# Optimization experiments

Hardware: AMD Instinct MI355X
Metric: run time of the kernel (lower is better)

## Reference

```python
import jax, jax.numpy as jnp
import numpy as np

NUM_HEADS = 16
DIM = 1280
HEAD_DIM = DIM // NUM_HEADS  # 80
N_TOKENS = 4096


def _rotate_half(x):
    x1, x2 = jnp.split(x, 2, axis=-1)
    return jnp.concatenate([-x2, x1], axis=-1)


def _apply_rotary_vision(t, freqs):
    # t: (N, H, D), freqs: (N, D//2)
    cos = jnp.tile(jnp.cos(freqs), (1, 2))[:, None, :]  # (N, 1, D)
    sin = jnp.tile(jnp.sin(freqs), (1, 2))[:, None, :]
    return t * cos + _rotate_half(t) * sin


def setup_inputs() -> dict:
    key = jax.random.key(0)
    ks = jax.random.split(key, 6)
    hidden_states = jax.random.normal(ks[0], (N_TOKENS, DIM), dtype=jnp.float32)
    # 4 packed variable-length image sequences
    cu_seqlens = jnp.array([0, 600, 1600, 2800, N_TOKENS], dtype=jnp.int32)
    rotary_pos_emb = jax.random.normal(ks[1], (N_TOKENS, HEAD_DIM // 2), dtype=jnp.float32)
    w_qkv = jax.random.normal(ks[2], (DIM, 3 * DIM), dtype=jnp.float32) * 0.02
    b_qkv = jax.random.normal(ks[3], (3 * DIM,), dtype=jnp.float32) * 0.02
    w_proj = jax.random.normal(ks[4], (DIM, DIM), dtype=jnp.float32) * 0.02
    b_proj = jax.random.normal(ks[5], (DIM,), dtype=jnp.float32) * 0.02
    return {"hidden_states": hidden_states, "cu_seqlens": cu_seqlens,
            "rotary_pos_emb": rotary_pos_emb, "w_qkv": w_qkv, "b_qkv": b_qkv,
            "w_proj": w_proj, "b_proj": b_proj}


def reference(hidden_states, cu_seqlens, rotary_pos_emb, w_qkv, b_qkv, w_proj, b_proj):
    N = hidden_states.shape[0]
    H, D = NUM_HEADS, HEAD_DIM
    qkv = hidden_states @ w_qkv + b_qkv                  # (N, 3*dim)
    qkv = qkv.reshape(N, 3, H, D)
    q, k, v = qkv[:, 0], qkv[:, 1], qkv[:, 2]            # (N, H, D)
    q = _apply_rotary_vision(q, rotary_pos_emb)
    k = _apply_rotary_vision(k, rotary_pos_emb)
    # segment id per token from cu_seqlens boundaries
    pos = jnp.arange(N, dtype=jnp.int32)
    seg = jnp.searchsorted(cu_seqlens, pos, side='right') - 1  # (N,)
    same_seg = seg[:, None] == seg[None, :]              # (N, N) bool
    scale = 1.0 / jnp.sqrt(jnp.asarray(D, dtype=q.dtype))
    scores = jnp.einsum('nhd,mhd->hnm', q, k) * scale    # (H, N, N)
    scores = jnp.where(same_seg[None, :, :], scores, jnp.finfo(scores.dtype).min)
    probs = jax.nn.softmax(scores, axis=-1)
    out = jnp.einsum('hnm,mhd->nhd', probs, v)           # (N, H, D)
    out = out.reshape(N, H * D)
    return out @ w_proj + b_proj
```

## Files before the change

### kernel.cpp

```cpp
#include <hip/hip_runtime.h>
#include <math.h>


#define N_TOK 4096
#define DIMM  1280
#define NHEAD 16
#define HD    80
#define QKVN  3840
#define KP    3840

typedef short bf16x8 __attribute__((ext_vector_type(8)));
typedef float f32x4  __attribute__((ext_vector_type(4)));

__device__ __forceinline__ unsigned short f2bf(float x) {
    unsigned int u = __float_as_uint(x);
    u += 0x7fff + ((u >> 16) & 1);
    return (unsigned short)(u >> 16);
}
__device__ __forceinline__ float bf2f(unsigned short h) {
    return __uint_as_float(((unsigned int)h) << 16);
}
__device__ __forceinline__ void gload_lds16(const void* g, void* l) {
    __builtin_amdgcn_global_load_lds(
        (const __attribute__((address_space(1))) unsigned int*)g,
        (__attribute__((address_space(3))) unsigned int*)l, 16, 0, 0);
}

#define MFMA16(a, b, c) __builtin_amdgcn_mfma_f32_16x16x32_bf16((a), (b), (c), 0, 0, 0)

__global__ void pack_A_kernel(const float* __restrict__ X, unsigned short* __restrict__ Ap)
{
    const int idx = blockIdx.x * blockDim.x + threadIdx.x;
    if (idx >= N_TOK * DIMM / 4) return;
    const int e = idx * 4;
    const int m = e / DIMM, k = e - (e / DIMM) * DIMM;
    const float4 v = *reinterpret_cast<const float4*>(&X[(size_t)m * DIMM + k]);
    ushort4 hi, lo;
    hi.x = f2bf(v.x); lo.x = f2bf(v.x - bf2f(hi.x));
    hi.y = f2bf(v.y); lo.y = f2bf(v.y - bf2f(hi.y));
    hi.z = f2bf(v.z); lo.z = f2bf(v.z - bf2f(hi.z));
    hi.w = f2bf(v.w); lo.w = f2bf(v.w - bf2f(hi.w));
    const size_t base = (size_t)m * KP + k;
    *reinterpret_cast<ushort4*>(&Ap[base])            = hi;
    *reinterpret_cast<ushort4*>(&Ap[base + DIMM])     = lo;
    *reinterpret_cast<ushort4*>(&Ap[base + 2 * DIMM]) = hi;
}

__global__ __launch_bounds__(256)
void pack_Bt_kernel(const float* __restrict__ W, unsigned short* __restrict__ Bt, int Ncols)
{
    __shared__ float Ts[32][33];
    const int k0 = blockIdx.x * 32, n0 = blockIdx.y * 32;
    const int t = threadIdx.x;
    const int r = t >> 3, c4 = (t & 7) * 4;
    const float4 v = *reinterpret_cast<const float4*>(&W[(size_t)(k0 + r) * Ncols + n0 + c4]);
    Ts[r][c4] = v.x; Ts[r][c4 + 1] = v.y; Ts[r][c4 + 2] = v.z; Ts[r][c4 + 3] = v.w;
    __syncthreads();
    float w0 = Ts[c4][r], w1 = Ts[c4 + 1][r], w2 = Ts[c4 + 2][r], w3 = Ts[c4 + 3][r];
    ushort4 hi, lo;
    hi.x = f2bf(w0); lo.x = f2bf(w0 - bf2f(hi.x));
    hi.y = f2bf(w1); lo.y = f2bf(w1 - bf2f(hi.y));
    hi.z = f2bf(w2); lo.z = f2bf(w2 - bf2f(hi.z));
    hi.w = f2bf(w3); lo.w = f2bf(w3 - bf2f(hi.w));
    const size_t base = (size_t)(n0 + r) * KP + k0 + c4;
    *reinterpret_cast<ushort4*>(&Bt[base])            = hi;
    *reinterpret_cast<ushort4*>(&Bt[base + DIMM])     = hi;
    *reinterpret_cast<ushort4*>(&Bt[base + 2 * DIMM]) = lo;
}

template<int EPI>
__global__ __launch_bounds__(256)
void gemm_mfma(const unsigned short* __restrict__ A, const unsigned short* __restrict__ Bt,
               const float* __restrict__ bias, float* __restrict__ out, int Ncols)
{
    __shared__ unsigned short As[128 * 32];
    __shared__ unsigned short Bs[128 * 32];

    const int tid  = threadIdx.x;
    const int w    = tid >> 6, lane = tid & 63;
    const int m0   = blockIdx.x * 128, n0 = blockIdx.y * 128;
    const int wm   = w >> 1, wn = w & 1;
    const int lm   = lane & 15, kb = lane >> 4;

    const char* Ag = (const char*)(A  + (size_t)(m0 + w * 32 + (lane >> 2)) * KP) + (lane & 3) * 16;
    const char* Bg = (const char*)(Bt + (size_t)(n0 + w * 32 + (lane >> 2)) * KP) + (lane & 3) * 16;
    char* AsB = (char*)As + w * 2048;
    char* BsB = (char*)Bs + w * 2048;
    const size_t rowskip = (size_t)16 * KP * 2;

    f32x4 acc[4][4] = {};

    for (int k0 = 0; k0 < KP; k0 += 32) {
        const size_t kb2 = (size_t)k0 * 2;
        gload_lds16(Ag + kb2,           AsB);
        gload_lds16(Ag + kb2 + rowskip, AsB + 1024);
        gload_lds16(Bg + kb2,           BsB);
        gload_lds16(Bg + kb2 + rowskip, BsB + 1024);
        __syncthreads();

        bf16x8 a[4], b[4];
        #pragma unroll
        for (int mf = 0; mf < 4; ++mf)
            a[mf] = *reinterpret_cast<const bf16x8*>(&As[(wm * 64 + mf * 16 + lm) * 32 + kb * 8]);
        #pragma unroll
        for (int nf = 0; nf < 4; ++nf)
            b[nf] = *reinterpret_cast<const bf16x8*>(&Bs[(wn * 64 + nf * 16 + lm) * 32 + kb * 8]);
        #pragma unroll
        for (int mf = 0; mf < 4; ++mf)
            #pragma unroll
            for (int nf = 0; nf < 4; ++nf)
                acc[mf][nf] = MFMA16(a[mf], b[nf], acc[mf][nf]);
        __syncthreads();
    }

    #pragma unroll
    for (int nf = 0; nf < 4; ++nf) {
        const int col = n0 + wn * 64 + nf * 16 + lm;
        const float bb = bias[col];
        #pragma unroll
        for (int mf = 0; mf < 4; ++mf) {
            #pragma unroll
            for (int r = 0; r < 4; ++r) {
                const int row = m0 + wm * 64 + mf * 16 + kb * 4 + r;
                const float c = acc[mf][nf][r] + bb;
                if (EPI == 0) {
                    out[(size_t)row * Ncols + col] = c;
                } else {
                    const int part = col / DIMM;
                    const int rem  = col - part * DIMM;
                    const int hh   = rem / HD;
                    const int d    = rem - hh * HD;
                    out[(((size_t)(part * NHEAD + hh)) * N_TOK + row) * HD + d] = c;
                }
            }
        }
    }
}

__global__ void rope_kernel(const float* __restrict__ freqs, float* __restrict__ q,
                            const float* __restrict__ k, unsigned short* __restrict__ Kp)
{
    const int idx = blockIdx.x * blockDim.x + threadIdx.x;
    if (idx >= N_TOK * NHEAD * 40) return;
    const int dp = idx % 40;
    const int t  = idx / 40;
    const int h  = t & 15;
    const int n  = t >> 4;

    const float f = freqs[n * 40 + dp];
    const float c = cosf(f);
    const float s = sinf(f);

    const size_t base = ((size_t)h * N_TOK + n) * HD;
    const float q1 = q[base + dp], q2 = q[base + dp + 40];
    q[base + dp]      = q1 * c - q2 * s;
    q[base + dp + 40] = q2 * c + q1 * s;

    const float scale = 0.11180339887498949f;
    const float k1 = k[base + dp], k2 = k[base + dp + 40];
    const float kr1 = (k1 * c - k2 * s) * scale;
    const float kr2 = (k2 * c + k1 * s) * scale;

    const size_t hi = ((size_t)(h * 2) * N_TOK + n) * 104;
    const size_t lo = ((size_t)(h * 2 + 1) * N_TOK + n) * 104;
    const unsigned short h1 = f2bf(kr1);
    Kp[hi + dp]      = h1;
    Kp[lo + dp]      = f2bf(kr1 - bf2f(h1));
    const unsigned short h2 = f2bf(kr2);
    Kp[hi + dp + 40] = h2;
    Kp[lo + dp + 40] = f2bf(kr2 - bf2f(h2));
    if (dp < 12) {
        Kp[hi + 80 + dp] = 0; Kp[hi + 92 + dp] = 0;
        Kp[lo + 80 + dp] = 0; Kp[lo + 92 + dp] = 0;
    }
}

__global__ __launch_bounds__(256)
void vpack_kernel(const float* __restrict__ v, unsigned short* __restrict__ Vt)
{
    __shared__ float T[32][81];
    const int t = blockIdx.x, h = blockIdx.y;
    const int kt = t * 32;
    for (int e = threadIdx.x; e < 32 * 80; e += 256) {
        const int key = e / 80, d = e - (e / 80) * 80;
        T[key][d] = v[((size_t)h * N_TOK + kt + key) * HD + d];
    }
    __syncthreads();
    unsigned short* base = Vt + ((size_t)h * 128 + t) * 6400;
    for (int e = threadIdx.x; e < 3200; e += 256) {
        const int d = e / 40, key = e - (e / 40) * 40;
        const float x = (key < 32) ? T[key][d] : 0.f;
        const unsigned short hi = f2bf(x);
        base[e]        = hi;
        base[3200 + e] = f2bf(x - bf2f(hi));
    }
}

__global__ __launch_bounds__(512, 2)
void attn_mfma(const float* __restrict__ qbuf, const unsigned short* __restrict__ Kp,
               const unsigned short* __restrict__ Vt, const int* __restrict__ cu,
               unsigned short* __restrict__ Ap)
{
    __shared__ __align__(16) unsigned short KhS[2][3328];
    __shared__ __align__(16) unsigned short KlS[2][3328];
    __shared__ __align__(16) unsigned short VS [2][6400];
    __shared__ __align__(16) unsigned short Pw [8][640];

    const int tid  = threadIdx.x;
    const int w    = tid >> 6, lane = tid & 63;
    const int lm   = lane & 15, g = lane >> 4;

    const int lin = blockIdx.x;
    const int h   = (lin & 7) * 2 + ((lin >> 3) & 1);
    const int q0  = (lin >> 4) * 128;

    const int c1 = cu[1], c2 = cu[2], c3 = cu[3];
    #define SEGOF(n) ((int)((n) >= c1) + (int)((n) >= c2) + (int)((n) >= c3))
    const int seg_first = SEGOF(q0);
    const int seg_last  = SEGOF(q0 + 127);
    const int cuv[5] = {0, c1, c2, c3, N_TOK};
    const int kmin = cuv[seg_first], kmax = cuv[seg_last + 1];
    const int kt0 = kmin & ~31;
    const int ntiles = (kmax - kt0 + 31) >> 5;

    const size_t hb = (size_t)h * N_TOK;

    bf16x8 qh[3], ql[3];
    {
        const int qrow = q0 + w * 16 + lm;
        const float* qp = qbuf + (hb + qrow) * HD;
        #pragma unroll
        for (int ks = 0; ks < 3; ++ks) {
            #pragma unroll
            for (int j = 0; j < 8; ++j) {
                const int d = ks * 32 + g * 8 + j;
                const float x = (d < HD) ? qp[d] : 0.f;
                const unsigned short hi = f2bf(x);
                qh[ks][j] = (short)hi;
                ql[ks][j] = (short)f2bf(x - bf2f(hi));
            }
        }
    }
    int qsg[4];
    #pragma unroll
    for (int r = 0; r < 4; ++r) qsg[r] = SEGOF(q0 + w * 16 + g * 4 + r);

    float mrun[4] = {-1e30f, -1e30f, -1e30f, -1e30f};
    float lrun[4] = {0.f, 0.f, 0.f, 0.f};
    f32x4 accO[5] = {};

    auto issue = [&](int buf, int kt) {
        const char* sK  = (const char*)(Kp + ((size_t)(h * 2)     * N_TOK + kt) * 104);
        const char* sKl = (const char*)(Kp + ((size_t)(h * 2 + 1) * N_TOK + kt) * 104);
        const char* sV  = (const char*)(Vt + ((size_t)h * 128 + (kt >> 5)) * 6400);
        char* dK  = (char*)&KhS[buf][0];
        char* dKl = (char*)&KlS[buf][0];
        char* dV  = (char*)&VS[buf][0];
        for (int j = w; j < 27; j += 8) {
            const char* s; char* d; int off; int half;
            if (j < 7)       { s = sK;  d = dK;  off = j * 1024;        half = (j == 6); }
            else if (j < 14) { s = sKl; d = dKl; off = (j - 7) * 1024;  half = (j == 13); }
            else             { s = sV;  d = dV;  off = (j - 14) * 1024; half = (j == 26); }
            if (!half || lane < 32)
                gload_lds16(s + off + (size_t)lane * 16, d + off);
        }
    };

    issue(0, kt0);
    __syncthreads();

    for (int ti = 0; ti < ntiles; ++ti) {
        const int kt  = kt0 + ti * 32;
        const int buf = ti & 1;
        if (ti + 1 < ntiles) issue(buf ^ 1, kt + 32);

        const unsigned short* Kh = &KhS[buf][0];
        const unsigned short* Kl = &KlS[buf][0];
        const unsigned short* Vb = &VS[buf][0];

        f32x4 s0 = {0.f, 0.f, 0.f, 0.f}, s1 = {0.f, 0.f, 0.f, 0.f};
        #pragma unroll
        for (int ks = 0; ks < 3; ++ks) {
            const bf16x8 k0h = *reinterpret_cast<const bf16x8*>(&Kh[lm * 104 + ks * 32 + g * 8]);
            const bf16x8 k0l = *reinterpret_cast<const bf16x8*>(&Kl[lm * 104 + ks * 32 + g * 8]);
            const bf16x8 k1h = *reinterpret_cast<const bf16x8*>(&Kh[(16 + lm) * 104 + ks * 32 + g * 8]);
            const bf16x8 k1l = *reinterpret_cast<const bf16x8*>(&Kl[(16 + lm) * 104 + ks * 32 + g * 8]);
            s0 = MFMA16(qh[ks], k0h, s0);
            s0 = MFMA16(ql[ks], k0h, s0);
            s0 = MFMA16(qh[ks], k0l, s0);
            s1 = MFMA16(qh[ks], k1h, s1);
            s1 = MFMA16(ql[ks], k1h, s1);
            s1 = MFMA16(qh[ks], k1l, s1);
        }

        const int ks0 = SEGOF(kt + lm), ks1 = SEGOF(kt + 16 + lm);
        float sfr[4], p0v[4], p1v[4];
        #pragma unroll
        for (int r = 0; r < 4; ++r) {
            const bool u0 = (ks0 == qsg[r]), u1 = (ks1 == qsg[r]);
            float v0 = u0 ? s0[r] : -1e30f;
            float v1 = u1 ? s1[r] : -1e30f;
            float tm = fmaxf(v0, v1);
            tm = fmaxf(tm, __shfl_xor(tm, 1));
            tm = fmaxf(tm, __shfl_xor(tm, 2));
            tm = fmaxf(tm, __shfl_xor(tm, 4));
            tm = fmaxf(tm, __shfl_xor(tm, 8));
            const float mo = mrun[r];
            const float mn = fmaxf(mo, tm);
            const float sc = __expf(mo - mn);
            const float e0 = u0 ? __expf(s0[r] - mn) : 0.f;
            const float e1 = u1 ? __expf(s1[r] - mn) : 0.f;
            float rs = e0 + e1;
            rs += __shfl_xor(rs, 1);
            rs += __shfl_xor(rs, 2);
            rs += __shfl_xor(rs, 4);
            rs += __shfl_xor(rs, 8);
            lrun[r] = lrun[r] * sc + rs;
            mrun[r] = mn;
            sfr[r] = sc; p0v[r] = e0; p1v[r] = e1;
        }
        #pragma unroll
        for (int r = 0; r < 4; ++r) {
            Pw[w][(g * 4 + r) * 40 + lm]      = f2bf(p0v[r]);
            Pw[w][(g * 4 + r) * 40 + 16 + lm] = f2bf(p1v[r]);
        }
        asm volatile("s_waitcnt lgkmcnt(0)" ::: "memory");
        __builtin_amdgcn_sched_barrier(0);

        const bf16x8 pa = *reinterpret_cast<const bf16x8*>(&Pw[w][lm * 40 + g * 8]);
        #pragma unroll
        for (int f = 0; f < 5; ++f) {
            const bf16x8 vh = *reinterpret_cast<const bf16x8*>(&Vb[(f * 16 + lm) * 40 + g * 8]);
            const bf16x8 vl = *reinterpret_cast<const bf16x8*>(&Vb[3200 + (f * 16 + lm) * 40 + g * 8]);
            f32x4 t = accO[f];
            t[0] *= sfr[0]; t[1] *= sfr[1]; t[2] *= sfr[2]; t[3] *= sfr[3];
            t = MFMA16(pa, vh, t);
            t = MFMA16(pa, vl, t);
            accO[f] = t;
        }

        __syncthreads();
    }

    #pragma unroll
    for (int r = 0; r < 4; ++r) {
        const float inv = 1.f / lrun[r];
        const int n = q0 + w * 16 + g * 4 + r;
        const size_t rb = (size_t)n * KP + h * HD;
        #pragma unroll
        for (int f = 0; f < 5; ++f) {
            const float v = accO[f][r] * inv;
            const unsigned short hi = f2bf(v);
            const unsigned short lo = f2bf(v - bf2f(hi));
            Ap[rb + f * 16 + lm]            = hi;
            Ap[rb + DIMM + f * 16 + lm]     = lo;
            Ap[rb + 2 * DIMM + f * 16 + lm] = hi;
        }
    }
    #undef SEGOF
}

extern "C" void kernel_launch(void* const* d_in, const int* in_sizes, int n_in,
                              void* d_out, int out_size, void* d_ws, size_t ws_size,
                              hipStream_t stream)
{
    const float* hidden = (const float*)d_in[0];
    const int*   cu     = (const int*)  d_in[1];
    const float* rope   = (const float*)d_in[2];
    const float* w_qkv  = (const float*)d_in[3];
    const float* b_qkv  = (const float*)d_in[4];
    const float* w_proj = (const float*)d_in[5];
    const float* b_proj = (const float*)d_in[6];
    float*       out    = (float*)d_out;

    const size_t perbuf = (size_t)NHEAD * N_TOK * HD;
    float* qbuf = (float*)d_ws;
    float* kbuf = qbuf + perbuf;
    float* vbuf = kbuf + perbuf;
    unsigned short* Apack = (unsigned short*)(vbuf + perbuf);
    unsigned short* BtQ   = Apack + (size_t)N_TOK * KP;
    unsigned short* BtP   = BtQ + (size_t)QKVN * KP;
    unsigned short* Vt    = BtP + (size_t)DIMM * KP;
    unsigned short* Kp    = BtQ;

    pack_A_kernel<<<(N_TOK * DIMM / 4 + 255) / 256, 256, 0, stream>>>(hidden, Apack);
    pack_Bt_kernel<<<dim3(DIMM / 32, QKVN / 32), 256, 0, stream>>>(w_qkv, BtQ, QKVN);
    pack_Bt_kernel<<<dim3(DIMM / 32, DIMM / 32), 256, 0, stream>>>(w_proj, BtP, DIMM);

    gemm_mfma<1><<<dim3(N_TOK / 128, QKVN / 128), 256, 0, stream>>>(Apack, BtQ, b_qkv, qbuf, QKVN);

    rope_kernel<<<(N_TOK * NHEAD * 40 + 255) / 256, 256, 0, stream>>>(rope, qbuf, kbuf, Kp);
    vpack_kernel<<<dim3(128, NHEAD), 256, 0, stream>>>(vbuf, Vt);

    attn_mfma<<<512, 512, 0, stream>>>(qbuf, Kp, Vt, cu, Apack);

    gemm_mfma<0><<<dim3(N_TOK / 128, DIMM / 128), 256, 0, stream>>>(Apack, BtP, b_proj, out, DIMM);
}
```

Baseline: 624.1 us.

## Transpose attention score MFMA, add lazy softmax rescale, and XCD-swizzle GEMM blocks

The attention kernel now computes S^T (K as the A operand), so each lane owns one query row. The row max and sum need only two cross-lane shuffles instead of four per row. It adds a deferred-rescale rule that skips the running-max update and accumulator scaling when the new tile max stays within 8 of the current max, and drops the occupancy hint of 2 from launch bounds. The GEMMs switch to a 1D grid with an XCD-aware block remap for better L2 locality. The trade-offs are extra shuffles to broadcast the scale factors back, and more register freedom at the possible cost of occupancy.

```diff
diff --git a/kernel.cpp b/kernel.cpp
--- a/kernel.cpp
+++ b/kernel.cpp
@@ -71,14 +71,19 @@
 template<int EPI>
 __global__ __launch_bounds__(256)
 void gemm_mfma(const unsigned short* __restrict__ A, const unsigned short* __restrict__ Bt,
-               const float* __restrict__ bias, float* __restrict__ out, int Ncols)
+               const float* __restrict__ bias, float* __restrict__ out, int Ncols, int nwg)
 {
     __shared__ unsigned short As[128 * 32];
     __shared__ unsigned short Bs[128 * 32];
 
     const int tid  = threadIdx.x;
     const int w    = tid >> 6, lane = tid & 63;
-    const int m0   = blockIdx.x * 128, n0 = blockIdx.y * 128;
+
+    const int lin = blockIdx.x;
+    const int wg  = (lin & 7) * (nwg >> 3) + (lin >> 3);
+    const int m0  = (wg & 31) * 128;
+    const int n0  = (wg >> 5) * 128;
+
     const int wm   = w >> 1, wn = w & 1;
     const int lm   = lane & 15, kb = lane >> 4;
 
@@ -196,7 +201,7 @@
     }
 }
 
-__global__ __launch_bounds__(512, 2)
+__global__ __launch_bounds__(512)
 void attn_mfma(const float* __restrict__ qbuf, const unsigned short* __restrict__ Kp,
                const unsigned short* __restrict__ Vt, const int* __restrict__ cu,
                unsigned short* __restrict__ Ap)
@@ -226,8 +231,8 @@
     const size_t hb = (size_t)h * N_TOK;
 
     bf16x8 qh[3], ql[3];
+    const int qrow = q0 + w * 16 + lm;
     {
-        const int qrow = q0 + w * 16 + lm;
         const float* qp = qbuf + (hb + qrow) * HD;
         #pragma unroll
         for (int ks = 0; ks < 3; ++ks) {
@@ -241,12 +246,10 @@
             }
         }
     }
-    int qsg[4];
-    #pragma unroll
-    for (int r = 0; r < 4; ++r) qsg[r] = SEGOF(q0 + w * 16 + g * 4 + r);
-
-    float mrun[4] = {-1e30f, -1e30f, -1e30f, -1e30f};
-    float lrun[4] = {0.f, 0.f, 0.f, 0.f};
+    const int sq  = SEGOF(qrow);
+    const int klo = cuv[sq], khi = cuv[sq + 1];
+
+    float mrow = -1e30f, lrow = 0.f;
     f32x4 accO[5] = {};
 
     auto issue = [&](int buf, int kt) {
@@ -285,44 +288,68 @@
             const bf16x8 k0l = *reinterpret_cast<const bf16x8*>(&Kl[lm * 104 + ks * 32 + g * 8]);
             const bf16x8 k1h = *reinterpret_cast<const bf16x8*>(&Kh[(16 + lm) * 104 + ks * 32 + g * 8]);
             const bf16x8 k1l = *reinterpret_cast<const bf16x8*>(&Kl[(16 + lm) * 104 + ks * 32 + g * 8]);
-            s0 = MFMA16(qh[ks], k0h, s0);
-            s0 = MFMA16(ql[ks], k0h, s0);
-            s0 = MFMA16(qh[ks], k0l, s0);
-            s1 = MFMA16(qh[ks], k1h, s1);
-            s1 = MFMA16(ql[ks], k1h, s1);
-            s1 = MFMA16(qh[ks], k1l, s1);
-        }
-
-        const int ks0 = SEGOF(kt + lm), ks1 = SEGOF(kt + 16 + lm);
-        float sfr[4], p0v[4], p1v[4];
+            s0 = MFMA16(k0h, qh[ks], s0);
+            s0 = MFMA16(k0h, ql[ks], s0);
+            s0 = MFMA16(k0l, qh[ks], s0);
+            s1 = MFMA16(k1h, qh[ks], s1);
+            s1 = MFMA16(k1h, ql[ks], s1);
+            s1 = MFMA16(k1l, qh[ks], s1);
+        }
+
+        bool v0m[4], v1m[4];
         #pragma unroll
         for (int r = 0; r < 4; ++r) {
-            const bool u0 = (ks0 == qsg[r]), u1 = (ks1 == qsg[r]);
-            float v0 = u0 ? s0[r] : -1e30f;
-            float v1 = u1 ? s1[r] : -1e30f;
-            float tm = fmaxf(v0, v1);
-            tm = fmaxf(tm, __shfl_xor(tm, 1));
-            tm = fmaxf(tm, __shfl_xor(tm, 2));
-            tm = fmaxf(tm, __shfl_xor(tm, 4));
-            tm = fmaxf(tm, __shfl_xor(tm, 8));
-            const float mo = mrun[r];
-            const float mn = fmaxf(mo, tm);
-            const float sc = __expf(mo - mn);
-            const float e0 = u0 ? __expf(s0[r] - mn) : 0.f;
-            const float e1 = u1 ? __expf(s1[r] - mn) : 0.f;
-            float rs = e0 + e1;
-            rs += __shfl_xor(rs, 1);
-            rs += __shfl_xor(rs, 2);
-            rs += __shfl_xor(rs, 4);
-            rs += __shfl_xor(rs, 8);
-            lrun[r] = lrun[r] * sc + rs;
-            mrun[r] = mn;
-            sfr[r] = sc; p0v[r] = e0; p1v[r] = e1;
-        }
+            const int j0 = kt + g * 4 + r;
+            const int j1 = j0 + 16;
+            v0m[r] = (j0 >= klo) && (j0 < khi);
+            v1m[r] = (j1 >= klo) && (j1 < khi);
+        }
+
+        float tm = -1e30f;
         #pragma unroll
         for (int r = 0; r < 4; ++r) {
-            Pw[w][(g * 4 + r) * 40 + lm]      = f2bf(p0v[r]);
-            Pw[w][(g * 4 + r) * 40 + 16 + lm] = f2bf(p1v[r]);
+            tm = fmaxf(tm, fmaxf(v0m[r] ? s0[r] : -1e30f, v1m[r] ? s1[r] : -1e30f));
+        }
+        tm = fmaxf(tm, __shfl_xor(tm, 16));
+        tm = fmaxf(tm, __shfl_xor(tm, 32));
+
+        const bool defer = __all(tm <= mrow + 8.0f);
+        if (!defer) {
+            const float mn = fmaxf(mrow, tm);
+            const float sc = __expf(mrow - mn);
+            mrow = mn;
+            lrow *= sc;
+            float scq[4];
+            #pragma unroll
+            for (int r = 0; r < 4; ++r) scq[r] = __shfl(sc, ((lane >> 4) << 2) + r);
+            #pragma unroll
+            for (int f = 0; f < 5; ++f) {
+                accO[f][0] *= scq[0]; accO[f][1] *= scq[1];
+                accO[f][2] *= scq[2]; accO[f][3] *= scq[3];
+            }
+        }
+
+        float p0[4], p1[4], rs = 0.f;
+        #pragma unroll
+        for (int r = 0; r < 4; ++r) {
+            p0[r] = v0m[r] ? __expf(s0[r] - mrow) : 0.f;
+            p1[r] = v1m[r] ? __expf(s1[r] - mrow) : 0.f;
+            rs += p0[r] + p1[r];
+        }
+        rs += __shfl_xor(rs, 16);
+        rs += __shfl_xor(rs, 32);
+        lrow += rs;
+
+        {
+            unsigned int u;
+            u = (unsigned int)f2bf(p0[0]) | ((unsigned int)f2bf(p0[1]) << 16);
+            *reinterpret_cast<unsigned int*>(&Pw[w][lm * 40 + g * 4])      = u;
+            u = (unsigned int)f2bf(p0[2]) | ((unsigned int)f2bf(p0[3]) << 16);
+            *reinterpret_cast<unsigned int*>(&Pw[w][lm * 40 + g * 4 + 2])  = u;
+            u = (unsigned int)f2bf(p1[0]) | ((unsigned int)f2bf(p1[1]) << 16);
+            *reinterpret_cast<unsigned int*>(&Pw[w][lm * 40 + 16 + g * 4]) = u;
+            u = (unsigned int)f2bf(p1[2]) | ((unsigned int)f2bf(p1[3]) << 16);
+            *reinterpret_cast<unsigned int*>(&Pw[w][lm * 40 + 18 + g * 4]) = u;
         }
         asm volatile("s_waitcnt lgkmcnt(0)" ::: "memory");
         __builtin_amdgcn_sched_barrier(0);
@@ -332,24 +359,25 @@
         for (int f = 0; f < 5; ++f) {
             const bf16x8 vh = *reinterpret_cast<const bf16x8*>(&Vb[(f * 16 + lm) * 40 + g * 8]);
             const bf16x8 vl = *reinterpret_cast<const bf16x8*>(&Vb[3200 + (f * 16 + lm) * 40 + g * 8]);
-            f32x4 t = accO[f];
-            t[0] *= sfr[0]; t[1] *= sfr[1]; t[2] *= sfr[2]; t[3] *= sfr[3];
-            t = MFMA16(pa, vh, t);
-            t = MFMA16(pa, vl, t);
-            accO[f] = t;
+            accO[f] = MFMA16(pa, vh, accO[f]);
+            accO[f] = MFMA16(pa, vl, accO[f]);
         }
 
         __syncthreads();
     }
+
+    const float linv = 1.f / lrow;
+    float invq[4];
+    #pragma unroll
+    for (int r = 0; r < 4; ++r) invq[r] = __shfl(linv, ((lane >> 4) << 2) + r);
 
     #pragma unroll
     for (int r = 0; r < 4; ++r) {
-        const float inv = 1.f / lrun[r];
         const int n = q0 + w * 16 + g * 4 + r;
         const size_t rb = (size_t)n * KP + h * HD;
         #pragma unroll
         for (int f = 0; f < 5; ++f) {
-            const float v = accO[f][r] * inv;
+            const float v = accO[f][r] * invq[r];
             const unsigned short hi = f2bf(v);
             const unsigned short lo = f2bf(v - bf2f(hi));
             Ap[rb + f * 16 + lm]            = hi;
@@ -387,12 +415,12 @@
     pack_Bt_kernel<<<dim3(DIMM / 32, QKVN / 32), 256, 0, stream>>>(w_qkv, BtQ, QKVN);
     pack_Bt_kernel<<<dim3(DIMM / 32, DIMM / 32), 256, 0, stream>>>(w_proj, BtP, DIMM);
 
-    gemm_mfma<1><<<dim3(N_TOK / 128, QKVN / 128), 256, 0, stream>>>(Apack, BtQ, b_qkv, qbuf, QKVN);
+    gemm_mfma<1><<<960, 256, 0, stream>>>(Apack, BtQ, b_qkv, qbuf, QKVN, 960);
 
     rope_kernel<<<(N_TOK * NHEAD * 40 + 255) / 256, 256, 0, stream>>>(rope, qbuf, kbuf, Kp);
     vpack_kernel<<<dim3(128, NHEAD), 256, 0, stream>>>(vbuf, Vt);
 
     attn_mfma<<<512, 512, 0, stream>>>(qbuf, Kp, Vt, cu, Apack);
 
-    gemm_mfma<0><<<dim3(N_TOK / 128, DIMM / 128), 256, 0, stream>>>(Apack, BtP, b_proj, out, DIMM);
-}
+    gemm_mfma<0><<<320, 256, 0, stream>>>(Apack, BtP, b_proj, out, DIMM, 320);
+}
```

After: 564.6 us. -9.5%, faster.
